# Kernel tuning notes

Measured on AMD Instinct MI355X. Metric: run time of the kernel, lower is better.

Reference implementation:

```python
import jax, jax.numpy as jnp
import numpy as np

B, S, D = 8, 2048, 512
LN_EPS = 1e-5

def _layernorm(x, gamma, beta):
    mu = jnp.mean(x, axis=-1, keepdims=True)
    var = jnp.mean(jnp.square(x - mu), axis=-1, keepdims=True)
    return (x - mu) * jax.lax.rsqrt(var + LN_EPS) * gamma + beta

def setup_inputs() -> dict:
    key = jax.random.key(0)
    ks = jax.random.split(key, 10)
    s_in = 1.0 / np.sqrt(2 * D)
    s_d = 1.0 / np.sqrt(D)
    return {
        "Noise_x": jax.random.normal(ks[0], (B, S, D), jnp.float32),
        "X": jax.random.normal(ks[1], (B, S, D), jnp.float32),
        "cond": jax.random.normal(ks[2], (B, S, D), jnp.float32),
        "W_gate": jax.random.normal(ks[3], (2 * D, D), jnp.float32) * s_in,
        "b_gate": jnp.zeros((D,), jnp.float32),
        "W1": jax.random.normal(ks[4], (D, 2 * D), jnp.float32) * s_d,
        "b1": jnp.zeros((2 * D,), jnp.float32),
        "W2": jax.random.normal(ks[5], (2 * D, D), jnp.float32) * s_in,
        "b2": jnp.zeros((D,), jnp.float32),
        "g1": jnp.ones((D,), jnp.float32),
        "be1": jnp.zeros((D,), jnp.float32),
        "g2": jnp.ones((D,), jnp.float32),
        "be2": jnp.zeros((D,), jnp.float32),
    }

def reference(Noise_x, X, cond, W_gate, b_gate, W1, b1, W2, b2, g1, be1, g2, be2):
    # gated fusion of noise and condition
    combined = jnp.concatenate([Noise_x, cond], axis=-1)            # [B,S,2D]
    gate = jax.nn.sigmoid(combined @ W_gate + b_gate)               # [B,S,D]
    fused = gate * Noise_x + (1.0 - gate) * cond                    # [B,S,D]
    # hand-rolled attention: Q = fused, K = V = X
    scale = 1.0 / jnp.sqrt(jnp.asarray(D, fused.dtype))
    scores = jnp.einsum('bqd,bkd->bqk', fused, X) * scale           # [B,S,S]
    attn = jax.nn.softmax(scores, axis=-1)
    attn_out = jnp.einsum('bqk,bkd->bqd', attn, X)                  # [B,S,D]
    # residual + norm, FFN (exact GELU as in torch default), residual + norm
    q = _layernorm(fused + attn_out, g1, be1)
    ff = jax.nn.gelu(q @ W1 + b1, approximate=False) @ W2 + b2
    return _layernorm(q + ff, g2, be2)
```

## Files before the change

### kernel.cpp

```cpp
#include <hip/hip_runtime.h>
#include <math.h>

typedef unsigned short ushort_t;
typedef unsigned int uint_t;
typedef __attribute__((ext_vector_type(8))) short short8;
typedef __attribute__((ext_vector_type(4))) float floatx4;

constexpr int B = 8;
constexpr int S = 2048;
constexpr int D = 512;
constexpr int BS = B * S;
constexpr float LN_EPS = 1e-5f;
constexpr float ATTN_SCALE = 0.04419417382415922f;


__device__ __forceinline__ ushort_t f2bf(float f) {
    union { float f; uint_t u; } x; x.f = f;
    uint_t r = x.u + 0x7fffu + ((x.u >> 16) & 1u);
    return (ushort_t)(r >> 16);
}
__device__ __forceinline__ float bf2f(ushort_t h) {
    union { uint_t u; float f; } y; y.u = ((uint_t)h) << 16;
    return y.f;
}
__device__ __forceinline__ short8 pack8(float4 a, float4 b) {
    short8 p;
    p[0] = (short)f2bf(a.x); p[1] = (short)f2bf(a.y);
    p[2] = (short)f2bf(a.z); p[3] = (short)f2bf(a.w);
    p[4] = (short)f2bf(b.x); p[5] = (short)f2bf(b.y);
    p[6] = (short)f2bf(b.z); p[7] = (short)f2bf(b.w);
    return p;
}

__device__ __forceinline__ float blk_reduce_sum(float v, float* sm) {
#pragma unroll
    for (int o = 32; o; o >>= 1) v += __shfl_down(v, o, 64);
    __syncthreads();
    if ((threadIdx.x & 63) == 0) sm[threadIdx.x >> 6] = v;
    __syncthreads();
    return sm[0] + sm[1] + sm[2] + sm[3];
}
__device__ __forceinline__ float blk_reduce_max(float v, float* sm) {
#pragma unroll
    for (int o = 32; o; o >>= 1) v = fmaxf(v, __shfl_down(v, o, 64));
    __syncthreads();
    if ((threadIdx.x & 63) == 0) sm[threadIdx.x >> 6] = v;
    __syncthreads();
    return fmaxf(fmaxf(sm[0], sm[1]), fmaxf(sm[2], sm[3]));
}

__global__ __launch_bounds__(256) void transpose_cvt(
    const float* __restrict__ in, ushort_t* __restrict__ out, int R, int C,
    ushort_t* __restrict__ out2) {
    __shared__ float tl[32][33];
    const size_t zoff = (size_t)blockIdx.z * R * C;
    const int tx = threadIdx.x & 31, ty = threadIdx.x >> 5;
    const int c0 = blockIdx.x * 32, r0 = blockIdx.y * 32;
#pragma unroll
    for (int i = 0; i < 4; i++) {
        const float v = in[zoff + (size_t)(r0 + ty + i * 8) * C + c0 + tx];
        tl[ty + i * 8][tx] = v;
        if (out2) out2[zoff + (size_t)(r0 + ty + i * 8) * C + c0 + tx] = f2bf(v);
    }
    __syncthreads();
#pragma unroll
    for (int i = 0; i < 4; i++)
        out[zoff + (size_t)(c0 + ty + i * 8) * R + r0 + tx] = f2bf(tl[tx][ty + i * 8]);
}

#define GEMM_PREAMBLE()                                                        \
    __shared__ ushort_t As[128 * 40];                                          \
    __shared__ ushort_t Bs[128 * 40];                                          \
    const int t = threadIdx.x;                                                 \
    const int m0 = blockIdx.y * 128, n0 = blockIdx.x * 128;                    \
    const int sr = t >> 2;                                          \
    const int sc = (t & 3) * 8;                                 \
    const int lane = t & 63, w = t >> 6;                                       \
    const int wm = (w >> 1) * 64, wn = (w & 1) * 64;                           \
    const int fr = lane & 15, fq = lane >> 4;                                  \
    floatx4 acc[4][4];                                                         \
    _Pragma("unroll") for (int i = 0; i < 4; i++)                              \
        _Pragma("unroll") for (int j = 0; j < 4; j++) {                        \
            acc[i][j][0] = 0.f; acc[i][j][1] = 0.f;                            \
            acc[i][j][2] = 0.f; acc[i][j][3] = 0.f; }

#define GEMM_MFMA_STAGE()                                                      \
    short8 af[4], bfg[4];                                                      \
    _Pragma("unroll") for (int i = 0; i < 4; i++) {                            \
        af[i]  = *(const short8*)&As[(wm + i * 16 + fr) * 40 + fq * 8];        \
        bfg[i] = *(const short8*)&Bs[(wn + i * 16 + fr) * 40 + fq * 8];        \
    }                                                                          \
    _Pragma("unroll") for (int i = 0; i < 4; i++)                              \
        _Pragma("unroll") for (int j = 0; j < 4; j++)                          \
            acc[i][j] = __builtin_amdgcn_mfma_f32_16x16x32_bf16(               \
                af[i], bfg[j], acc[i][j], 0, 0, 0);

__global__ __launch_bounds__(256) void gate_gemm(
    const float* __restrict__ NX, const float* __restrict__ CD,
    const ushort_t* __restrict__ WgT, const float* __restrict__ bg,
    ushort_t* __restrict__ Fb) {
    GEMM_PREAMBLE();
    const ushort_t* Bb = WgT + (size_t)n0 * 1024;

    float4 f00, f01, f10, f11;
    int4 b0, b1;
    {
        const float* p0 = NX + (size_t)(m0 + sr) * 512 + sc;
        const float* p1 = NX + (size_t)(m0 + sr + 64) * 512 + sc;
        f00 = *(const float4*)p0;  f01 = *(const float4*)(p0 + 4);
        f10 = *(const float4*)p1;  f11 = *(const float4*)(p1 + 4);
        b0 = *(const int4*)(Bb + (size_t)sr * 1024 + sc);
        b1 = *(const int4*)(Bb + (size_t)(sr + 64) * 1024 + sc);
    }

    for (int k0 = 0; k0 < 1024; k0 += 32) {
        __syncthreads();
        short8 pa0 = pack8(f00, f01), pa1 = pack8(f10, f11);
        *(short8*)&As[sr * 40 + sc] = pa0;
        *(short8*)&As[(sr + 64) * 40 + sc] = pa1;
        *(int4*)&Bs[sr * 40 + sc] = b0;
        *(int4*)&Bs[(sr + 64) * 40 + sc] = b1;
        __syncthreads();
        const int kn = k0 + 32;
        if (kn < 1024) {
            const float* Asrc = (kn < 512) ? NX : CD;
            const int kk = kn & 511;
            const float* p0 = Asrc + (size_t)(m0 + sr) * 512 + kk + sc;
            const float* p1 = Asrc + (size_t)(m0 + sr + 64) * 512 + kk + sc;
            f00 = *(const float4*)p0;  f01 = *(const float4*)(p0 + 4);
            f10 = *(const float4*)p1;  f11 = *(const float4*)(p1 + 4);
            b0 = *(const int4*)(Bb + (size_t)sr * 1024 + kn + sc);
            b1 = *(const int4*)(Bb + (size_t)(sr + 64) * 1024 + kn + sc);
        }
        GEMM_MFMA_STAGE();
    }

#pragma unroll
    for (int i = 0; i < 4; i++) {
#pragma unroll
        for (int j = 0; j < 4; j++) {
#pragma unroll
            for (int r = 0; r < 4; r++) {
                const int m = m0 + wm + i * 16 + fq * 4 + r;
                const int n = n0 + wn + j * 16 + fr;
                const float z = acc[i][j][r] + bg[n];
                const float g = 1.f / (1.f + expf(-z));
                const size_t idx = (size_t)m * 512 + n;
                Fb[idx] = f2bf(g * NX[idx] + (1.f - g) * CD[idx]);
            }
        }
    }
}

#define GEMM3_PREAMBLE()                                                       \
    __shared__ ushort_t As[128 * 40];                                          \
    __shared__ ushort_t Bs[64 * 40];                                           \
    const int t = threadIdx.x;                                                 \
    const int m0 = blockIdx.y * 128, n0 = blockIdx.x * 64;                     \
    const int sr = t >> 2;                                          \
    const int sc = (t & 3) * 8;                                 \
    const int lane = t & 63, w = t >> 6;                                       \
    const int wm = w * 32;                                                     \
    const int fr = lane & 15, fq = lane >> 4;                                  \
    floatx4 acc[2][4];                                                         \
    _Pragma("unroll") for (int i = 0; i < 2; i++)                              \
        _Pragma("unroll") for (int j = 0; j < 4; j++) {                        \
            acc[i][j][0] = 0.f; acc[i][j][1] = 0.f;                            \
            acc[i][j][2] = 0.f; acc[i][j][3] = 0.f; }

#define GEMM3_MFMA_STAGE()                                                     \
    short8 af[2], bfg[4];                                                      \
    _Pragma("unroll") for (int i = 0; i < 2; i++)                              \
        af[i]  = *(const short8*)&As[(wm + i * 16 + fr) * 40 + fq * 8];        \
    _Pragma("unroll") for (int j = 0; j < 4; j++)                              \
        bfg[j] = *(const short8*)&Bs[(j * 16 + fr) * 40 + fq * 8];             \
    _Pragma("unroll") for (int i = 0; i < 2; i++)                              \
        _Pragma("unroll") for (int j = 0; j < 4; j++)                          \
            acc[i][j] = __builtin_amdgcn_mfma_f32_16x16x32_bf16(               \
                af[i], bfg[j], acc[i][j], 0, 0, 0);

template <int EPI>
__global__ __launch_bounds__(256) void gemm3_std(
    const ushort_t* __restrict__ A, int lda, long sAz,
    const ushort_t* __restrict__ Bt, int ldb, long sBz,
    void* __restrict__ Cv, int ldc, long sCz,
    int K, const float* __restrict__ bias, float scale, int init) {
    GEMM3_PREAMBLE();
    const ushort_t* Ab = A + (size_t)blockIdx.z * sAz + (size_t)m0 * lda;
    const ushort_t* Bb = Bt + (size_t)blockIdx.z * sBz + (size_t)n0 * ldb;

    int4 a0 = *(const int4*)(Ab + (size_t)sr * lda + sc);
    int4 a1 = *(const int4*)(Ab + (size_t)(sr + 64) * lda + sc);
    int4 b0 = *(const int4*)(Bb + (size_t)sr * ldb + sc);

    for (int k0 = 0; k0 < K; k0 += 32) {
        __syncthreads();
        *(int4*)&As[sr * 40 + sc] = a0;
        *(int4*)&As[(sr + 64) * 40 + sc] = a1;
        *(int4*)&Bs[sr * 40 + sc] = b0;
        __syncthreads();
        const int kn = k0 + 32;
        if (kn < K) {
            a0 = *(const int4*)(Ab + (size_t)sr * lda + kn + sc);
            a1 = *(const int4*)(Ab + (size_t)(sr + 64) * lda + kn + sc);
            b0 = *(const int4*)(Bb + (size_t)sr * ldb + kn + sc);
        }
        GEMM3_MFMA_STAGE();
    }

#pragma unroll
    for (int i = 0; i < 2; i++) {
#pragma unroll
        for (int j = 0; j < 4; j++) {
#pragma unroll
            for (int r = 0; r < 4; r++) {
                const int m = m0 + wm + i * 16 + fq * 4 + r;
                const int n = n0 + j * 16 + fr;
                float v = acc[i][j][r];
                if (EPI == 0) {
                    ushort_t* C = (ushort_t*)Cv + (size_t)blockIdx.z * sCz;
                    C[(size_t)m * ldc + n] = f2bf(v * scale);
                } else if (EPI == 1) {
                    const float x = v + bias[n];
                    const float gl = 0.5f * x * (1.f + erff(x * 0.70710678118654752f));
                    ushort_t* C = (ushort_t*)Cv;
                    C[(size_t)m * ldc + n] = f2bf(gl);
                } else {
                    float* T = (float*)Cv;
                    const size_t idx = (size_t)m * ldc + n;
                    T[idx] = T[idx] + v + (init ? bias[n] : 0.f);
                }
            }
        }
    }
}

__global__ __launch_bounds__(256) void softmax_bf16(ushort_t* __restrict__ Sc) {
    __shared__ float sm[4];
    ushort_t* row = Sc + (size_t)blockIdx.x * 2048;
    const int t = threadIdx.x;
    ushort_t raw[8];
    *(int4*)raw = *(const int4*)(row + t * 8);
    float e[8];
    float mx = -1e30f;
#pragma unroll
    for (int j = 0; j < 8; j++) { e[j] = bf2f(raw[j]); mx = fmaxf(mx, e[j]); }
    mx = blk_reduce_max(mx, sm);
    float s = 0.f;
#pragma unroll
    for (int j = 0; j < 8; j++) { e[j] = expf(e[j] - mx); s += e[j]; }
    s = blk_reduce_sum(s, sm);
    const float inv = 1.f / s;
#pragma unroll
    for (int j = 0; j < 8; j++) raw[j] = f2bf(e[j] * inv);
    *(int4*)(row + t * 8) = *(const int4*)raw;
}

__global__ __launch_bounds__(256) void ln1_kernel(
    const ushort_t* __restrict__ Fb, const ushort_t* __restrict__ Ab,
    const float* __restrict__ g1, const float* __restrict__ be1,
    float* __restrict__ qf, ushort_t* __restrict__ qb) {
    __shared__ float sm[4];
    const size_t base = (size_t)blockIdx.x * 512;
    const int t = threadIdx.x;
    const float v0 = bf2f(Fb[base + t]) + bf2f(Ab[base + t]);
    const float v1 = bf2f(Fb[base + t + 256]) + bf2f(Ab[base + t + 256]);
    const float mu = blk_reduce_sum(v0 + v1, sm) * (1.f / 512.f);
    const float d0 = v0 - mu, d1 = v1 - mu;
    const float var = blk_reduce_sum(d0 * d0 + d1 * d1, sm) * (1.f / 512.f);
    const float rs = rsqrtf(var + LN_EPS);
    const float y0 = d0 * rs * g1[t] + be1[t];
    const float y1 = d1 * rs * g1[t + 256] + be1[t + 256];
    qf[base + t] = y0;          qf[base + t + 256] = y1;
    qb[base + t] = f2bf(y0);    qb[base + t + 256] = f2bf(y1);
}

__global__ __launch_bounds__(256) void ln2_kernel(
    float* __restrict__ T, const float* __restrict__ g,
    const float* __restrict__ be) {
    __shared__ float sm[4];
    const size_t base = (size_t)blockIdx.x * 512;
    const int t = threadIdx.x;
    const float v0 = T[base + t];
    const float v1 = T[base + t + 256];
    const float mu = blk_reduce_sum(v0 + v1, sm) * (1.f / 512.f);
    const float d0 = v0 - mu, d1 = v1 - mu;
    const float var = blk_reduce_sum(d0 * d0 + d1 * d1, sm) * (1.f / 512.f);
    const float rs = rsqrtf(var + LN_EPS);
    T[base + t] = d0 * rs * g[t] + be[t];
    T[base + t + 256] = d1 * rs * g[t + 256] + be[t + 256];
}

extern "C" void kernel_launch(void* const* d_in, const int* in_sizes, int n_in,
                              void* d_out, int out_size, void* d_ws, size_t ws_size,
                              hipStream_t stream) {
    const float* NX  = (const float*)d_in[0];
    const float* X   = (const float*)d_in[1];
    const float* CD  = (const float*)d_in[2];
    const float* Wg  = (const float*)d_in[3];
    const float* bg  = (const float*)d_in[4];
    const float* W1  = (const float*)d_in[5];
    const float* b1  = (const float*)d_in[6];
    const float* W2  = (const float*)d_in[7];
    const float* b2  = (const float*)d_in[8];
    const float* g1  = (const float*)d_in[9];
    const float* be1 = (const float*)d_in[10];
    const float* g2  = (const float*)d_in[11];
    const float* be2 = (const float*)d_in[12];

    ushort_t* slot0 = (ushort_t*)d_ws;
    ushort_t* slot1 = (ushort_t*)((char*)d_ws + 16777216);
    ushort_t* slot2 = (ushort_t*)((char*)d_ws + 33554432);
    ushort_t* Xb    = slot0;
    ushort_t* attnb = slot0;
    ushort_t* hbuf  = slot0;
    ushort_t* Fb    = slot1;
    ushort_t* W1T   = slot1;
    ushort_t* W2T   = slot1 + 524288;
    ushort_t* WgT   = slot2;
    ushort_t* XbT   = slot2;
    ushort_t* qb    = slot2;
    ushort_t* Scb   = (ushort_t*)d_out;
    float*    qf    = (float*)d_out;

    transpose_cvt<<<dim3(512 / 32, 1024 / 32, 1), 256, 0, stream>>>(
        Wg, WgT, 1024, 512, nullptr);

    gate_gemm<<<dim3(4, 128), 256, 0, stream>>>(NX, CD, WgT, bg, Fb);

    transpose_cvt<<<dim3(512 / 32, 2048 / 32, 8), 256, 0, stream>>>(
        X, XbT, 2048, 512, Xb);

    for (int g = 0; g < 2; g++) {
        const size_t go = (size_t)g * 4 * S * 512;
        gemm3_std<0><<<dim3(32, 16, 4), 256, 0, stream>>>(
            Fb + go, D, (long)S * D,
            Xb + go, D, (long)S * D,
            (void*)Scb, S, (long)S * S, D, nullptr, ATTN_SCALE, 0);
        softmax_bf16<<<4 * S, 256, 0, stream>>>(Scb);
        gemm3_std<0><<<dim3(8, 16, 4), 256, 0, stream>>>(
            Scb, S, (long)S * S,
            XbT + go, S, (long)D * S,
            (void*)(attnb + go), 512, (long)S * 512, S, nullptr, 1.f, 0);
    }

    ln1_kernel<<<BS, 256, 0, stream>>>(Fb, attnb, g1, be1, qf, qb);

    transpose_cvt<<<dim3(1024 / 32, 512 / 32, 1), 256, 0, stream>>>(
        W1, W1T, 512, 1024, nullptr);
    transpose_cvt<<<dim3(512 / 32, 1024 / 32, 1), 256, 0, stream>>>(
        W2, W2T, 1024, 512, nullptr);

    for (int h = 0; h < 2; h++) {
        gemm3_std<1><<<dim3(8, 128), 256, 0, stream>>>(
            qb, 512, 0, W1T + (size_t)h * 512 * 512, 512, 0,
            (void*)hbuf, 512, 0, 512, b1 + h * 512, 1.f, 0);
        gemm3_std<2><<<dim3(8, 128), 256, 0, stream>>>(
            hbuf, 512, 0, W2T + h * 512, 1024, 0,
            (void*)qf, 512, 0, 512, b2, 1.f, h == 0 ? 1 : 0);
    }

    ln2_kernel<<<BS, 256, 0, stream>>>(qf, g2, be2);
}
```

Baseline: 545.3 us.

## Double-buffer LDS in all GEMMs and use 128x128 tiles for scores and FFN

Every GEMM kernel now keeps two LDS stages, so the next K-slice is written into the alternate buffer while MFMAs run on the current one. This drops one of the two barriers per iteration. A new gemm2_std kernel with 128x128 tiles and a 2x2 warp layout replaces the 128x64 kernel for the QK^T scores GEMM and both FFN GEMMs. That raises per-block data reuse, at the cost of twice the LDS and more accumulator registers, which may reduce occupancy.

```diff
diff --git a/kernel.cpp b/kernel.cpp
--- a/kernel.cpp
+++ b/kernel.cpp
@@ -68,38 +68,56 @@
         out[zoff + (size_t)(c0 + ty + i * 8) * R + r0 + tx] = f2bf(tl[tx][ty + i * 8]);
 }
 
-#define GEMM_PREAMBLE()                                                        \
-    __shared__ ushort_t As[128 * 40];                                          \
-    __shared__ ushort_t Bs[128 * 40];                                          \
+#define IDX128()                                                               \
     const int t = threadIdx.x;                                                 \
-    const int m0 = blockIdx.y * 128, n0 = blockIdx.x * 128;                    \
     const int sr = t >> 2;                                          \
     const int sc = (t & 3) * 8;                                 \
     const int lane = t & 63, w = t >> 6;                                       \
-    const int wm = (w >> 1) * 64, wn = (w & 1) * 64;                           \
-    const int fr = lane & 15, fq = lane >> 4;                                  \
-    floatx4 acc[4][4];                                                         \
-    _Pragma("unroll") for (int i = 0; i < 4; i++)                              \
-        _Pragma("unroll") for (int j = 0; j < 4; j++) {                        \
-            acc[i][j][0] = 0.f; acc[i][j][1] = 0.f;                            \
-            acc[i][j][2] = 0.f; acc[i][j][3] = 0.f; }
-
-#define GEMM_MFMA_STAGE()                                                      \
-    short8 af[4], bfg[4];                                                      \
-    _Pragma("unroll") for (int i = 0; i < 4; i++) {                            \
-        af[i]  = *(const short8*)&As[(wm + i * 16 + fr) * 40 + fq * 8];        \
-        bfg[i] = *(const short8*)&Bs[(wn + i * 16 + fr) * 40 + fq * 8];        \
-    }                                                                          \
-    _Pragma("unroll") for (int i = 0; i < 4; i++)                              \
+    const int fr = lane & 15, fq = lane >> 4;
+
+#define MFMA16(Asp, Bsp)                                                       \
+    {                                                                          \
+        short8 af[4], bfg[4];                                                  \
+        _Pragma("unroll") for (int i = 0; i < 4; i++) {                        \
+            af[i]  = *(const short8*)&(Asp)[(wm + i * 16 + fr) * 40 + fq * 8]; \
+            bfg[i] = *(const short8*)&(Bsp)[(wn + i * 16 + fr) * 40 + fq * 8]; \
+        }                                                                      \
+        _Pragma("unroll") for (int i = 0; i < 4; i++)                          \
+            _Pragma("unroll") for (int j = 0; j < 4; j++)                      \
+                acc[i][j] = __builtin_amdgcn_mfma_f32_16x16x32_bf16(           \
+                    af[i], bfg[j], acc[i][j], 0, 0, 0);                        \
+    }
+
+#define MFMA8(Asp, Bsp)                                                        \
+    {                                                                          \
+        short8 af[2], bfg[4];                                                  \
+        _Pragma("unroll") for (int i = 0; i < 2; i++)                          \
+            af[i]  = *(const short8*)&(Asp)[(wm + i * 16 + fr) * 40 + fq * 8]; \
         _Pragma("unroll") for (int j = 0; j < 4; j++)                          \
-            acc[i][j] = __builtin_amdgcn_mfma_f32_16x16x32_bf16(               \
-                af[i], bfg[j], acc[i][j], 0, 0, 0);
+            bfg[j] = *(const short8*)&(Bsp)[(j * 16 + fr) * 40 + fq * 8];      \
+        _Pragma("unroll") for (int i = 0; i < 2; i++)                          \
+            _Pragma("unroll") for (int j = 0; j < 4; j++)                      \
+                acc[i][j] = __builtin_amdgcn_mfma_f32_16x16x32_bf16(           \
+                    af[i], bfg[j], acc[i][j], 0, 0, 0);                        \
+    }
 
 __global__ __launch_bounds__(256) void gate_gemm(
     const float* __restrict__ NX, const float* __restrict__ CD,
     const ushort_t* __restrict__ WgT, const float* __restrict__ bg,
     ushort_t* __restrict__ Fb) {
-    GEMM_PREAMBLE();
+    __shared__ ushort_t As[2][128 * 40];
+    __shared__ ushort_t Bs[2][128 * 40];
+    IDX128();
+    const int m0 = blockIdx.y * 128, n0 = blockIdx.x * 128;
+    const int wm = (w >> 1) * 64, wn = (w & 1) * 64;
+    floatx4 acc[4][4];
+#pragma unroll
+    for (int i = 0; i < 4; i++)
+#pragma unroll
+        for (int j = 0; j < 4; j++) {
+            acc[i][j][0] = 0.f; acc[i][j][1] = 0.f;
+            acc[i][j][2] = 0.f; acc[i][j][3] = 0.f;
+        }
     const ushort_t* Bb = WgT + (size_t)n0 * 1024;
 
     float4 f00, f01, f10, f11;
@@ -111,28 +129,44 @@
         f10 = *(const float4*)p1;  f11 = *(const float4*)(p1 + 4);
         b0 = *(const int4*)(Bb + (size_t)sr * 1024 + sc);
         b1 = *(const int4*)(Bb + (size_t)(sr + 64) * 1024 + sc);
-    }
-
+        *(short8*)&As[0][sr * 40 + sc] = pack8(f00, f01);
+        *(short8*)&As[0][(sr + 64) * 40 + sc] = pack8(f10, f11);
+        *(int4*)&Bs[0][sr * 40 + sc] = b0;
+        *(int4*)&Bs[0][(sr + 64) * 40 + sc] = b1;
+    }
+    {
+        const float* p0 = NX + (size_t)(m0 + sr) * 512 + 32 + sc;
+        const float* p1 = NX + (size_t)(m0 + sr + 64) * 512 + 32 + sc;
+        f00 = *(const float4*)p0;  f01 = *(const float4*)(p0 + 4);
+        f10 = *(const float4*)p1;  f11 = *(const float4*)(p1 + 4);
+        b0 = *(const int4*)(Bb + (size_t)sr * 1024 + 32 + sc);
+        b1 = *(const int4*)(Bb + (size_t)(sr + 64) * 1024 + 32 + sc);
+    }
+    __syncthreads();
+
+    int cur = 0;
     for (int k0 = 0; k0 < 1024; k0 += 32) {
-        __syncthreads();
-        short8 pa0 = pack8(f00, f01), pa1 = pack8(f10, f11);
-        *(short8*)&As[sr * 40 + sc] = pa0;
-        *(short8*)&As[(sr + 64) * 40 + sc] = pa1;
-        *(int4*)&Bs[sr * 40 + sc] = b0;
-        *(int4*)&Bs[(sr + 64) * 40 + sc] = b1;
-        __syncthreads();
+        MFMA16(As[cur], Bs[cur]);
         const int kn = k0 + 32;
         if (kn < 1024) {
-            const float* Asrc = (kn < 512) ? NX : CD;
-            const int kk = kn & 511;
-            const float* p0 = Asrc + (size_t)(m0 + sr) * 512 + kk + sc;
-            const float* p1 = Asrc + (size_t)(m0 + sr + 64) * 512 + kk + sc;
-            f00 = *(const float4*)p0;  f01 = *(const float4*)(p0 + 4);
-            f10 = *(const float4*)p1;  f11 = *(const float4*)(p1 + 4);
-            b0 = *(const int4*)(Bb + (size_t)sr * 1024 + kn + sc);
-            b1 = *(const int4*)(Bb + (size_t)(sr + 64) * 1024 + kn + sc);
-        }
-        GEMM_MFMA_STAGE();
+            *(short8*)&As[cur ^ 1][sr * 40 + sc] = pack8(f00, f01);
+            *(short8*)&As[cur ^ 1][(sr + 64) * 40 + sc] = pack8(f10, f11);
+            *(int4*)&Bs[cur ^ 1][sr * 40 + sc] = b0;
+            *(int4*)&Bs[cur ^ 1][(sr + 64) * 40 + sc] = b1;
+            const int kf = kn + 32;
+            if (kf < 1024) {
+                const float* Asrc = (kf < 512) ? NX : CD;
+                const int kk = kf & 511;
+                const float* p0 = Asrc + (size_t)(m0 + sr) * 512 + kk + sc;
+                const float* p1 = Asrc + (size_t)(m0 + sr + 64) * 512 + kk + sc;
+                f00 = *(const float4*)p0;  f01 = *(const float4*)(p0 + 4);
+                f10 = *(const float4*)p1;  f11 = *(const float4*)(p1 + 4);
+                b0 = *(const int4*)(Bb + (size_t)sr * 1024 + kf + sc);
+                b1 = *(const int4*)(Bb + (size_t)(sr + 64) * 1024 + kf + sc);
+            }
+        }
+        __syncthreads();
+        cur ^= 1;
     }
 
 #pragma unroll
@@ -152,32 +186,91 @@
     }
 }
 
-#define GEMM3_PREAMBLE()                                                       \
-    __shared__ ushort_t As[128 * 40];                                          \
-    __shared__ ushort_t Bs[64 * 40];                                           \
-    const int t = threadIdx.x;                                                 \
-    const int m0 = blockIdx.y * 128, n0 = blockIdx.x * 64;                     \
-    const int sr = t >> 2;                                          \
-    const int sc = (t & 3) * 8;                                 \
-    const int lane = t & 63, w = t >> 6;                                       \
-    const int wm = w * 32;                                                     \
-    const int fr = lane & 15, fq = lane >> 4;                                  \
-    floatx4 acc[2][4];                                                         \
-    _Pragma("unroll") for (int i = 0; i < 2; i++)                              \
-        _Pragma("unroll") for (int j = 0; j < 4; j++) {                        \
-            acc[i][j][0] = 0.f; acc[i][j][1] = 0.f;                            \
-            acc[i][j][2] = 0.f; acc[i][j][3] = 0.f; }
-
-#define GEMM3_MFMA_STAGE()                                                     \
-    short8 af[2], bfg[4];                                                      \
-    _Pragma("unroll") for (int i = 0; i < 2; i++)                              \
-        af[i]  = *(const short8*)&As[(wm + i * 16 + fr) * 40 + fq * 8];        \
-    _Pragma("unroll") for (int j = 0; j < 4; j++)                              \
-        bfg[j] = *(const short8*)&Bs[(j * 16 + fr) * 40 + fq * 8];             \
-    _Pragma("unroll") for (int i = 0; i < 2; i++)                              \
-        _Pragma("unroll") for (int j = 0; j < 4; j++)                          \
-            acc[i][j] = __builtin_amdgcn_mfma_f32_16x16x32_bf16(               \
-                af[i], bfg[j], acc[i][j], 0, 0, 0);
+template <int EPI>
+__global__ __launch_bounds__(256) void gemm2_std(
+    const ushort_t* __restrict__ A, int lda, long sAz,
+    const ushort_t* __restrict__ Bt, int ldb, long sBz,
+    void* __restrict__ Cv, int ldc, long sCz,
+    int K, const float* __restrict__ bias, float scale, int init) {
+    __shared__ ushort_t As[2][128 * 40];
+    __shared__ ushort_t Bs[2][128 * 40];
+    IDX128();
+    const int m0 = blockIdx.y * 128, n0 = blockIdx.x * 128;
+    const int wm = (w >> 1) * 64, wn = (w & 1) * 64;
+    floatx4 acc[4][4];
+#pragma unroll
+    for (int i = 0; i < 4; i++)
+#pragma unroll
+        for (int j = 0; j < 4; j++) {
+            acc[i][j][0] = 0.f; acc[i][j][1] = 0.f;
+            acc[i][j][2] = 0.f; acc[i][j][3] = 0.f;
+        }
+    const ushort_t* Ab = A + (size_t)blockIdx.z * sAz + (size_t)m0 * lda;
+    const ushort_t* Bb = Bt + (size_t)blockIdx.z * sBz + (size_t)n0 * ldb;
+
+    int4 a0 = *(const int4*)(Ab + (size_t)sr * lda + sc);
+    int4 a1 = *(const int4*)(Ab + (size_t)(sr + 64) * lda + sc);
+    int4 b0 = *(const int4*)(Bb + (size_t)sr * ldb + sc);
+    int4 b1 = *(const int4*)(Bb + (size_t)(sr + 64) * ldb + sc);
+    *(int4*)&As[0][sr * 40 + sc] = a0;
+    *(int4*)&As[0][(sr + 64) * 40 + sc] = a1;
+    *(int4*)&Bs[0][sr * 40 + sc] = b0;
+    *(int4*)&Bs[0][(sr + 64) * 40 + sc] = b1;
+    if (32 < K) {
+        a0 = *(const int4*)(Ab + (size_t)sr * lda + 32 + sc);
+        a1 = *(const int4*)(Ab + (size_t)(sr + 64) * lda + 32 + sc);
+        b0 = *(const int4*)(Bb + (size_t)sr * ldb + 32 + sc);
+        b1 = *(const int4*)(Bb + (size_t)(sr + 64) * ldb + 32 + sc);
+    }
+    __syncthreads();
+
+    int cur = 0;
+    for (int k0 = 0; k0 < K; k0 += 32) {
+        MFMA16(As[cur], Bs[cur]);
+        const int kn = k0 + 32;
+        if (kn < K) {
+            *(int4*)&As[cur ^ 1][sr * 40 + sc] = a0;
+            *(int4*)&As[cur ^ 1][(sr + 64) * 40 + sc] = a1;
+            *(int4*)&Bs[cur ^ 1][sr * 40 + sc] = b0;
+            *(int4*)&Bs[cur ^ 1][(sr + 64) * 40 + sc] = b1;
+            const int kf = kn + 32;
+            if (kf < K) {
+                a0 = *(const int4*)(Ab + (size_t)sr * lda + kf + sc);
+                a1 = *(const int4*)(Ab + (size_t)(sr + 64) * lda + kf + sc);
+                b0 = *(const int4*)(Bb + (size_t)sr * ldb + kf + sc);
+                b1 = *(const int4*)(Bb + (size_t)(sr + 64) * ldb + kf + sc);
+            }
+        }
+        __syncthreads();
+        cur ^= 1;
+    }
+
+#pragma unroll
+    for (int i = 0; i < 4; i++) {
+#pragma unroll
+        for (int j = 0; j < 4; j++) {
+#pragma unroll
+            for (int r = 0; r < 4; r++) {
+                const int m = m0 + wm + i * 16 + fq * 4 + r;
+                const int n = n0 + wn + j * 16 + fr;
+                float v = acc[i][j][r];
+                if (EPI == 0) {
+                    ushort_t* C = (ushort_t*)Cv + (size_t)blockIdx.z * sCz;
+                    C[(size_t)m * ldc + n] = f2bf(v * scale);
+                } else if (EPI == 1) {
+                    const float x = v + bias[n];
+                    const float gl = 0.5f * x * (1.f + erff(x * 0.70710678118654752f));
+                    ushort_t* C = (ushort_t*)Cv;
+                    C[(size_t)m * ldc + n] = f2bf(gl);
+                } else {
+                    float* T = (float*)Cv;
+                    const size_t idx = (size_t)m * ldc + n;
+                    T[idx] = T[idx] + v + (init ? bias[n] : 0.f);
+                }
+            }
+        }
+    }
+}
 
 template <int EPI>
 __global__ __launch_bounds__(256) void gemm3_std(
@@ -185,27 +278,52 @@
     const ushort_t* __restrict__ Bt, int ldb, long sBz,
     void* __restrict__ Cv, int ldc, long sCz,
     int K, const float* __restrict__ bias, float scale, int init) {
-    GEMM3_PREAMBLE();
+    __shared__ ushort_t As[2][128 * 40];
+    __shared__ ushort_t Bs[2][64 * 40];
+    IDX128();
+    const int m0 = blockIdx.y * 128, n0 = blockIdx.x * 64;
+    const int wm = w * 32;
+    floatx4 acc[2][4];
+#pragma unroll
+    for (int i = 0; i < 2; i++)
+#pragma unroll
+        for (int j = 0; j < 4; j++) {
+            acc[i][j][0] = 0.f; acc[i][j][1] = 0.f;
+            acc[i][j][2] = 0.f; acc[i][j][3] = 0.f;
+        }
     const ushort_t* Ab = A + (size_t)blockIdx.z * sAz + (size_t)m0 * lda;
     const ushort_t* Bb = Bt + (size_t)blockIdx.z * sBz + (size_t)n0 * ldb;
 
     int4 a0 = *(const int4*)(Ab + (size_t)sr * lda + sc);
     int4 a1 = *(const int4*)(Ab + (size_t)(sr + 64) * lda + sc);
     int4 b0 = *(const int4*)(Bb + (size_t)sr * ldb + sc);
-
+    *(int4*)&As[0][sr * 40 + sc] = a0;
+    *(int4*)&As[0][(sr + 64) * 40 + sc] = a1;
+    *(int4*)&Bs[0][sr * 40 + sc] = b0;
+    if (32 < K) {
+        a0 = *(const int4*)(Ab + (size_t)sr * lda + 32 + sc);
+        a1 = *(const int4*)(Ab + (size_t)(sr + 64) * lda + 32 + sc);
+        b0 = *(const int4*)(Bb + (size_t)sr * ldb + 32 + sc);
+    }
+    __syncthreads();
+
+    int cur = 0;
     for (int k0 = 0; k0 < K; k0 += 32) {
-        __syncthreads();
-        *(int4*)&As[sr * 40 + sc] = a0;
-        *(int4*)&As[(sr + 64) * 40 + sc] = a1;
-        *(int4*)&Bs[sr * 40 + sc] = b0;
-        __syncthreads();
+        MFMA8(As[cur], Bs[cur]);
         const int kn = k0 + 32;
         if (kn < K) {
-            a0 = *(const int4*)(Ab + (size_t)sr * lda + kn + sc);
-            a1 = *(const int4*)(Ab + (size_t)(sr + 64) * lda + kn + sc);
-            b0 = *(const int4*)(Bb + (size_t)sr * ldb + kn + sc);
-        }
-        GEMM3_MFMA_STAGE();
+            *(int4*)&As[cur ^ 1][sr * 40 + sc] = a0;
+            *(int4*)&As[cur ^ 1][(sr + 64) * 40 + sc] = a1;
+            *(int4*)&Bs[cur ^ 1][sr * 40 + sc] = b0;
+            const int kf = kn + 32;
+            if (kf < K) {
+                a0 = *(const int4*)(Ab + (size_t)sr * lda + kf + sc);
+                a1 = *(const int4*)(Ab + (size_t)(sr + 64) * lda + kf + sc);
+                b0 = *(const int4*)(Bb + (size_t)sr * ldb + kf + sc);
+            }
+        }
+        __syncthreads();
+        cur ^= 1;
     }
 
 #pragma unroll
@@ -333,7 +451,7 @@
 
     for (int g = 0; g < 2; g++) {
         const size_t go = (size_t)g * 4 * S * 512;
-        gemm3_std<0><<<dim3(32, 16, 4), 256, 0, stream>>>(
+        gemm2_std<0><<<dim3(16, 16, 4), 256, 0, stream>>>(
             Fb + go, D, (long)S * D,
             Xb + go, D, (long)S * D,
             (void*)Scb, S, (long)S * S, D, nullptr, ATTN_SCALE, 0);
@@ -352,10 +470,10 @@
         W2, W2T, 1024, 512, nullptr);
 
     for (int h = 0; h < 2; h++) {
-        gemm3_std<1><<<dim3(8, 128), 256, 0, stream>>>(
+        gemm2_std<1><<<dim3(4, 128), 256, 0, stream>>>(
             qb, 512, 0, W1T + (size_t)h * 512 * 512, 512, 0,
             (void*)hbuf, 512, 0, 512, b1 + h * 512, 1.f, 0);
-        gemm3_std<2><<<dim3(8, 128), 256, 0, stream>>>(
+        gemm2_std<2><<<dim3(4, 128), 256, 0, stream>>>(
             hbuf, 512, 0, W2T + h * 512, 1024, 0,
             (void*)qf, 512, 0, 512, b2, 1.f, h == 0 ? 1 : 0);
     }
```

New measurement: 539.0 us. Within noise of the previous version (-1.2%).
